# Kernel tuning notes

Measured on AMD Instinct MI355X. Metric: run time of the kernel, lower is better.

## Reference

```python
import jax, jax.numpy as jnp
import numpy as np

B, T, E, A = 512, 64, 1024, 32
S, D, H = 30, 200, 200          # stoch, deter, hidden
SS = D + S                      # state_size = 230
MIN_STD = 0.1
UPDATE_BIAS = -1.0
W_SCALE = 0.05


def setup_inputs() -> dict:
    key = jax.random.key(0)
    ks = jax.random.split(key, 17)
    n = jax.random.normal
    return {
        "embed":       n(ks[0], (B, T, E), jnp.float32),
        "action":      n(ks[1], (B, T, A), jnp.float32),
        "context":     n(ks[2], (B, T, SS), jnp.float32),
        "noise_prior": n(ks[3], (T, B, S), jnp.float32),
        "noise_post":  n(ks[4], (T, B, S), jnp.float32),
        "w_inp":       n(ks[5], (S + SS + A, H), jnp.float32) * W_SCALE,
        "b_inp":       jnp.zeros((H,), jnp.float32),
        "w_gru":       n(ks[6], (H + D, 3 * D), jnp.float32) * W_SCALE,
        "b_gru":       jnp.zeros((3 * D,), jnp.float32),
        "w_img_out":   n(ks[7], (D, H), jnp.float32) * W_SCALE,
        "b_img_out":   jnp.zeros((H,), jnp.float32),
        "w_obs_out":   n(ks[8], (D + E, H), jnp.float32) * W_SCALE,
        "b_obs_out":   jnp.zeros((H,), jnp.float32),
        "w_ims_stat":  n(ks[9], (H, 2 * S), jnp.float32) * W_SCALE,
        "b_ims_stat":  jnp.zeros((2 * S,), jnp.float32),
        "w_obs_stat":  n(ks[10], (H, 2 * S), jnp.float32) * W_SCALE,
        "b_obs_stat":  jnp.zeros((2 * S,), jnp.float32),
    }


def _observe(embed, action, context, noise_prior, noise_post,
             w_inp, b_inp, w_gru, b_gru, w_img_out, b_img_out,
             w_obs_out, b_obs_out, w_ims_stat, b_ims_stat,
             w_obs_stat, b_obs_stat):
    # time-major
    emb_t = jnp.swapaxes(embed, 0, 1)    # [T,B,E]
    act_t = jnp.swapaxes(action, 0, 1)   # [T,B,A]
    ctx_t = jnp.swapaxes(context, 0, 1)  # [T,B,SS]

    def step(carry, xs):
        stoch, deter = carry
        ctx, act, emb, n_p, n_o = xs
        # img_step: input MLP + GRU cell
        x = jnp.concatenate([stoch, ctx, act], -1)
        x = jax.nn.elu(x @ w_inp + b_inp)
        parts = jnp.concatenate([x, deter], -1) @ w_gru + b_gru
        reset, cand, update = jnp.split(parts, 3, -1)
        reset = jax.nn.sigmoid(reset)
        cand = jnp.tanh(reset * cand)
        update = jax.nn.sigmoid(update + UPDATE_BIAS)
        deter_new = update * cand + (1.0 - update) * deter
        # prior stats
        h = jax.nn.elu(deter_new @ w_img_out + b_img_out)
        st = h @ w_ims_stat + b_ims_stat
        pm, ps = jnp.split(st, 2, -1)
        ps = jax.nn.softplus(ps) + MIN_STD
        p_stoch = pm + ps * n_p
        # posterior stats
        ho = jax.nn.elu(jnp.concatenate([deter_new, emb], -1) @ w_obs_out + b_obs_out)
        so = ho @ w_obs_stat + b_obs_stat
        om, os_ = jnp.split(so, 2, -1)
        os_ = jax.nn.softplus(os_) + MIN_STD
        o_stoch = om + os_ * n_o
        out = jnp.concatenate([om, os_, o_stoch, pm, ps, p_stoch, deter_new], -1)
        return (o_stoch, deter_new), out

    carry0 = (jnp.zeros((B, S), embed.dtype), jnp.zeros((B, D), embed.dtype))
    _, ys = jax.lax.scan(step, carry0, (ctx_t, act_t, emb_t, noise_prior, noise_post))
    # ys: [T,B,6S+D] -> [B,T,6S+D]  (post mean/std/stoch, prior mean/std/stoch, deter)
    return jnp.swapaxes(ys, 0, 1)


def reference(embed, action, context, noise_prior, noise_post,
              w_inp, b_inp, w_gru, b_gru, w_img_out, b_img_out,
              w_obs_out, b_obs_out, w_ims_stat, b_ims_stat,
              w_obs_stat, b_obs_stat):
    return _observe(embed, action, context, noise_prior, noise_post,
                    w_inp, b_inp, w_gru, b_gru, w_img_out, b_img_out,
                    w_obs_out, b_obs_out, w_ims_stat, b_ims_stat,
                    w_obs_stat, b_obs_stat)
```

## Files before the change

kernel.cpp:

```cpp
#include <hip/hip_runtime.h>
#include <cstddef>

typedef short short8 __attribute__((ext_vector_type(8)));
typedef float f32x4 __attribute__((ext_vector_type(4)));
typedef unsigned short u16;

#define Bn 512
#define Tn 64
#define En 1024
#define An 32
#define Sn 30
#define Dn 200
#define Hn 200
#define SSn 230
#define OUTC 380

#define U16_WINP  0
#define EL_WINP   66560
#define U16_WGRU  66560
#define EL_WGRU   252928
#define U16_WIMG  319488
#define EL_WIMG   46592
#define U16_WOBSD 366080
#define EL_WOBSD  46592
#define U16_WIMS  412672
#define EL_WIMS   14336
#define U16_WOBSS 427008
#define EL_WOBSS  14336
#define U16_WOBSE 441344
#define EL_WOBSE  212992
#define U16_TOTAL 654336
#define PREOBS_BYTE_OFF 1308672

#define DEV static __device__ __forceinline__

DEV u16 f2bf(float f) {
  union { float f; unsigned u; } v; v.f = f;
  return (u16)((v.u + 0x7FFFu + ((v.u >> 16) & 1u)) >> 16);
}
DEV float bf2f(u16 h) {
  union { unsigned u; float f; } v; v.u = ((unsigned)h) << 16; return v.f;
}
DEV float elu1(float x)  { return x > 0.f ? x : expm1f(x); }
DEV float sigm(float x)  { return 1.f / (1.f + expf(-x)); }
DEV float splus(float x) { return x > 20.f ? x : log1pf(expf(x)); }

DEV void pack_one(const float* src, u16* dst, int li, int KT,
                  int Kr, int Nr, int ldN, int roff) {
  int j = li & 7, lane = (li >> 3) & 63, frag = li >> 9;
  int kt = frag % KT, nt = frag / KT;
  int k = kt * 32 + ((lane >> 4) << 3) + j;
  int n = nt * 16 + (lane & 15);
  float v = (k < Kr && n < Nr) ? src[(size_t)(k + roff) * ldN + n] : 0.f;
  dst[li] = f2bf(v);
}

__global__ __launch_bounds__(256) void k_pack(
    const float* w_inp, const float* w_gru, const float* w_img,
    const float* w_obs, const float* w_ims, const float* w_obss,
    u16* ws) {
  int idx = blockIdx.x * 256 + threadIdx.x;
  if (idx < U16_WGRU)       pack_one(w_inp,  ws + U16_WINP,  idx - U16_WINP, 10, 292, 200, 200, 0);
  else if (idx < U16_WIMG)  pack_one(w_gru,  ws + U16_WGRU,  idx - U16_WGRU, 13, 400, 600, 600, 0);
  else if (idx < U16_WOBSD) pack_one(w_img,  ws + U16_WIMG,  idx - U16_WIMG,  7, 200, 200, 200, 0);
  else if (idx < U16_WIMS)  pack_one(w_obs,  ws + U16_WOBSD, idx - U16_WOBSD, 7, 200, 200, 200, 0);
  else if (idx < U16_WOBSS) pack_one(w_ims,  ws + U16_WIMS,  idx - U16_WIMS,  7, 200,  60,  60, 0);
  else if (idx < U16_WOBSE) pack_one(w_obss, ws + U16_WOBSS, idx - U16_WOBSS, 7, 200,  60,  60, 0);
  else if (idx < U16_TOTAL) pack_one(w_obs,  ws + U16_WOBSE, idx - U16_WOBSE, 32, 1024, 200, 200, 200);
}

__global__ __launch_bounds__(256) void k_preobs(
    const float* __restrict__ emb, const u16* __restrict__ ws,
    float* __restrict__ pre) {
  __shared__ u16 Asm[64 * 72];
  __shared__ short8 Bsm[26 * 64];
  const short8* Wp = (const short8*)(ws + U16_WOBSE);

  int tid = threadIdx.x, wv = tid >> 6, lane = tid & 63;
  int lrow = lane & 15, quad = lane >> 4;
  int m0 = blockIdx.x * 64;
  int t = m0 >> 9, brow0 = m0 & 511;

  f32x4 acc[13];
  const f32x4 z4 = {0.f, 0.f, 0.f, 0.f};
#pragma unroll
  for (int i = 0; i < 13; ++i) acc[i] = z4;

  for (int kc = 0; kc < 16; ++kc) {
    __syncthreads();
#pragma unroll
    for (int q = 0; q < 4; ++q) {
      int i = tid + q * 256;
      int row = i >> 4, c4 = i & 15;
      const float* src = emb + ((size_t)((brow0 + row) * Tn + t)) * En + kc * 64 + c4 * 4;
      float4 v = *(const float4*)src;
      union { u16 h[4]; unsigned long long ll; } p;
      p.h[0] = f2bf(v.x); p.h[1] = f2bf(v.y); p.h[2] = f2bf(v.z); p.h[3] = f2bf(v.w);
      *(unsigned long long*)&Asm[row * 72 + c4 * 4] = p.ll;
    }
    for (int q = 0; q < 7; ++q) {
      int i = tid + q * 256;
      if (i < 1664) {
        int pair = i >> 6, l = i & 63;
        int ktl = pair / 13, nt = pair % 13;
        Bsm[i] = Wp[(nt * 32 + kc * 2 + ktl) * 64 + l];
      }
    }
    __syncthreads();
#pragma unroll
    for (int ktl = 0; ktl < 2; ++ktl) {
      short8 a = *(const short8*)&Asm[(wv * 16 + lrow) * 72 + ktl * 32 + quad * 8];
#pragma unroll
      for (int nt = 0; nt < 13; ++nt)
        acc[nt] = __builtin_amdgcn_mfma_f32_16x16x32_bf16(a, Bsm[(ktl * 13 + nt) * 64 + lane], acc[nt], 0, 0, 0);
    }
  }
#pragma unroll
  for (int nt = 0; nt < 13; ++nt) {
    int col = nt * 16 + lrow;
    if (col < 200) {
#pragma unroll
      for (int r = 0; r < 4; ++r) {
        int m = m0 + wv * 16 + quad * 4 + r;
        pre[(size_t)m * 200 + col] = acc[nt][r];
      }
    }
  }
}

__global__ __launch_bounds__(512, 2) void k_scan(
    const float* __restrict__ g_ctx, const float* __restrict__ g_act,
    const float* __restrict__ g_np, const float* __restrict__ g_no,
    const float* __restrict__ b_inp, const float* __restrict__ b_gru,
    const float* __restrict__ b_img, const float* __restrict__ b_obs,
    const float* __restrict__ b_ims, const float* __restrict__ b_obss,
    const u16* __restrict__ ws, const float* __restrict__ pre,
    float* __restrict__ out) {

  __shared__ u16 gin[16 * 424];
  __shared__ u16 U[16 * 616];
  __shared__ u16 hA[16 * 232];
  __shared__ u16 hoA[16 * 232];
  __shared__ float stp[16 * 66];
  __shared__ float sto[16 * 66];

  const short8* Winp  = (const short8*)(ws + U16_WINP);
  const short8* Wgru  = (const short8*)(ws + U16_WGRU);
  const short8* Wimg  = (const short8*)(ws + U16_WIMG);
  const short8* Wobsd = (const short8*)(ws + U16_WOBSD);
  const short8* Wims  = (const short8*)(ws + U16_WIMS);
  const short8* Wobss = (const short8*)(ws + U16_WOBSS);

  int tid = threadIdx.x, wv = tid >> 6, lane = tid & 63;
  int lrow = lane & 15, quad = lane >> 4;
  int b0 = blockIdx.x * 16;
  const f32x4 z4 = {0.f, 0.f, 0.f, 0.f};

  for (int i = tid; i < 16 * 424; i += 512) gin[i] = 0;
  for (int i = tid; i < 16 * 616; i += 512) U[i] = 0;
  for (int i = tid; i < 16 * 232; i += 512) { hA[i] = 0; hoA[i] = 0; }
  __syncthreads();

  for (int t = 0; t < Tn; ++t) {
    {
      int row = tid >> 5, sub = tid & 31;
      const float* crow = g_ctx + ((size_t)(b0 + row) * Tn + t) * SSn;
      for (int i = sub; i < SSn; i += 32) U[row * 328 + 30 + i] = f2bf(crow[i]);
      const float* arow = g_act + ((size_t)(b0 + row) * Tn + t) * An;
      if (sub < An) U[row * 328 + 260 + sub] = f2bf(arow[sub]);
      if (sub < 28) U[row * 328 + 292 + sub] = 0;
    }
    __syncthreads();

    for (int nt = wv; nt < 13; nt += 8) {
      f32x4 acc = z4;
      const short8* bp = Winp + (size_t)(nt * 10) * 64 + lane;
#pragma unroll
      for (int kt = 0; kt < 10; ++kt) {
        short8 a = *(const short8*)&U[lrow * 328 + kt * 32 + quad * 8];
        acc = __builtin_amdgcn_mfma_f32_16x16x32_bf16(a, bp[kt * 64], acc, 0, 0, 0);
      }
      int col = nt * 16 + lrow;
      if (col < 200) {
        float bias = b_inp[col];
#pragma unroll
        for (int r = 0; r < 4; ++r)
          gin[(quad * 4 + r) * 424 + col] = f2bf(elu1(acc[r] + bias));
      }
    }
    __syncthreads();

    for (int nt = wv; nt < 38; nt += 8) {
      f32x4 acc = z4;
      const short8* bp = Wgru + (size_t)(nt * 13) * 64 + lane;
#pragma unroll
      for (int kt = 0; kt < 13; ++kt) {
        short8 a = *(const short8*)&gin[lrow * 424 + kt * 32 + quad * 8];
        acc = __builtin_amdgcn_mfma_f32_16x16x32_bf16(a, bp[kt * 64], acc, 0, 0, 0);
      }
      int col = nt * 16 + lrow;
      if (col < 600) {
        float bias = b_gru[col];
#pragma unroll
        for (int r = 0; r < 4; ++r)
          U[(quad * 4 + r) * 616 + col] = f2bf(acc[r] + bias);
      }
    }
    __syncthreads();

    for (int i = tid; i < 16 * Dn; i += 512) {
      int row = i / Dn, d = i % Dn;
      float rg = bf2f(U[row * 616 + d]);
      float cg = bf2f(U[row * 616 + 200 + d]);
      float ug = bf2f(U[row * 616 + 400 + d]);
      float dold = bf2f(gin[row * 424 + 200 + d]);
      float rs  = sigm(rg);
      float cnd = tanhf(rs * cg);
      float up  = sigm(ug - 1.f);
      float dn  = up * cnd + (1.f - up) * dold;
      gin[row * 424 + 200 + d] = f2bf(dn);
      __builtin_nontemporal_store(dn, &out[((size_t)(b0 + row) * Tn + t) * OUTC + 180 + d]);
    }
    __syncthreads();

    for (int j = wv; j < 26; j += 8) {
      bool isobs = j >= 13;
      int nt = isobs ? j - 13 : j;
      const short8* bp = (isobs ? Wobsd : Wimg) + (size_t)(nt * 7) * 64 + lane;
      f32x4 acc = z4;
#pragma unroll
      for (int kt = 0; kt < 7; ++kt) {
        short8 a = *(const short8*)&gin[lrow * 424 + 200 + kt * 32 + quad * 8];
        acc = __builtin_amdgcn_mfma_f32_16x16x32_bf16(a, bp[kt * 64], acc, 0, 0, 0);
      }
      int col = nt * 16 + lrow;
      if (col < 200) {
        if (!isobs) {
          float bias = b_img[col];
#pragma unroll
          for (int r = 0; r < 4; ++r)
            hA[(quad * 4 + r) * 232 + col] = f2bf(elu1(acc[r] + bias));
        } else {
          float bias = b_obs[col];
#pragma unroll
          for (int r = 0; r < 4; ++r) {
            int row = quad * 4 + r;
            float po = pre[((size_t)t * Bn + b0 + row) * 200 + col];
            hoA[row * 232 + col] = f2bf(elu1(acc[r] + bias + po));
          }
        }
      }
    }
    __syncthreads();

    {
      bool isobs = wv >= 4;
      int nt = wv & 3;
      const short8* bp = (isobs ? Wobss : Wims) + (size_t)(nt * 7) * 64 + lane;
      const u16* src = isobs ? hoA : hA;
      f32x4 acc = z4;
#pragma unroll
      for (int kt = 0; kt < 7; ++kt) {
        short8 a = *(const short8*)&src[lrow * 232 + kt * 32 + quad * 8];
        acc = __builtin_amdgcn_mfma_f32_16x16x32_bf16(a, bp[kt * 64], acc, 0, 0, 0);
      }
      int col = nt * 16 + lrow;
      if (col < 60) {
        float bias = (isobs ? b_obss : b_ims)[col];
        float* dst = isobs ? sto : stp;
#pragma unroll
        for (int r = 0; r < 4; ++r)
          dst[(quad * 4 + r) * 66 + col] = acc[r] + bias;
      }
    }
    __syncthreads();

    if (tid < 480) {
      int row = tid / 30, s = tid % 30;
      size_t ob = ((size_t)(b0 + row) * Tn + t) * OUTC;
      size_t ni = ((size_t)t * Bn + b0 + row) * Sn + s;
      float pm = stp[row * 66 + s];
      float ps = splus(stp[row * 66 + 30 + s]) + 0.1f;
      float pst = pm + ps * g_np[ni];
      float om = sto[row * 66 + s];
      float os = splus(sto[row * 66 + 30 + s]) + 0.1f;
      float ost = om + os * g_no[ni];
      __builtin_nontemporal_store(om,  &out[ob + s]);
      __builtin_nontemporal_store(os,  &out[ob + 30 + s]);
      __builtin_nontemporal_store(ost, &out[ob + 60 + s]);
      __builtin_nontemporal_store(pm,  &out[ob + 90 + s]);
      __builtin_nontemporal_store(ps,  &out[ob + 120 + s]);
      __builtin_nontemporal_store(pst, &out[ob + 150 + s]);
      U[row * 328 + s] = f2bf(ost);
    }
    __syncthreads();
  }
}

extern "C" void kernel_launch(void* const* d_in, const int* in_sizes, int n_in,
                              void* d_out, int out_size, void* d_ws, size_t ws_size,
                              hipStream_t stream) {
  (void)in_sizes; (void)n_in; (void)out_size; (void)ws_size;
  const float* emb    = (const float*)d_in[0];
  const float* action = (const float*)d_in[1];
  const float* ctx    = (const float*)d_in[2];
  const float* np_    = (const float*)d_in[3];
  const float* no_    = (const float*)d_in[4];
  const float* w_inp  = (const float*)d_in[5];
  const float* b_inp  = (const float*)d_in[6];
  const float* w_gru  = (const float*)d_in[7];
  const float* b_gru  = (const float*)d_in[8];
  const float* w_img  = (const float*)d_in[9];
  const float* b_img  = (const float*)d_in[10];
  const float* w_obs  = (const float*)d_in[11];
  const float* b_obs  = (const float*)d_in[12];
  const float* w_ims  = (const float*)d_in[13];
  const float* b_ims  = (const float*)d_in[14];
  const float* w_obss = (const float*)d_in[15];
  const float* b_obss = (const float*)d_in[16];

  u16*   wsu = (u16*)d_ws;
  float* pre = (float*)((char*)d_ws + PREOBS_BYTE_OFF);
  float* out = (float*)d_out;

  k_pack<<<2556, 256, 0, stream>>>(w_inp, w_gru, w_img, w_obs, w_ims, w_obss, wsu);
  k_preobs<<<512, 256, 0, stream>>>(emb, wsu, pre);
  k_scan<<<32, 512, 0, stream>>>(ctx, action, np_, no_,
                                 b_inp, b_gru, b_img, b_obs, b_ims, b_obss,
                                 wsu, pre, out);
}
```

Before: 1.486 ms.

## Keep scan weights register-resident, fuse GRU gates into MFMA epilogue, prefetch inputs

The recurrent scan kernel now runs 16 waves per block. Each wave loads its slice of every weight matrix into registers once, instead of re-reading the packed weights from global memory at every timestep. The GRU weight packing is interleaved so one wave computes the reset, candidate and update tiles for the same columns, and the gate math runs in the MFMA epilogue, removing the shared-memory gate buffer and a separate elementwise pass. Next-step context and action, noise values and the precomputed observation terms are prefetched into registers early in each step. The trailing barrier is also dropped. The cost is very high register pressure, which risks spills, and several extra barriers per step.

New measurement: 2.572 ms. 73.1% more time.

```diff
diff --git a/kernel.cpp b/kernel.cpp
--- a/kernel.cpp
+++ b/kernel.cpp
@@ -16,23 +16,25 @@
 #define OUTC 380
 
 #define U16_WINP  0
-#define EL_WINP   66560
 #define U16_WGRU  66560
-#define EL_WGRU   252928
-#define U16_WIMG  319488
-#define EL_WIMG   46592
-#define U16_WOBSD 366080
-#define EL_WOBSD  46592
-#define U16_WIMS  412672
-#define EL_WIMS   14336
-#define U16_WOBSS 427008
-#define EL_WOBSS  14336
-#define U16_WOBSE 441344
-#define EL_WOBSE  212992
-#define U16_TOTAL 654336
-#define PREOBS_BYTE_OFF 1308672
+#define U16_WIMG  326144
+#define U16_WOBSD 372736
+#define U16_WIMS  419328
+#define U16_WOBSS 433664
+#define U16_WOBSE 448000
+#define U16_TOTAL 660992
+#define PREOBS_BYTE_OFF 1321984
+
+#define WINP8  0
+#define WGRU8  8320
+#define WIMG8  40768
+#define WOBSD8 46592
+#define WIMS8  52416
+#define WOBSS8 54208
+#define WOBSE8 56000
 
 #define DEV static __device__ __forceinline__
+#define MFMA(a,b,c) __builtin_amdgcn_mfma_f32_16x16x32_bf16((a),(b),(c),0,0,0)
 
 DEV u16 f2bf(float f) {
   union { float f; unsigned u; } v; v.f = f;
@@ -60,13 +62,24 @@
     const float* w_obs, const float* w_ims, const float* w_obss,
     u16* ws) {
   int idx = blockIdx.x * 256 + threadIdx.x;
-  if (idx < U16_WGRU)       pack_one(w_inp,  ws + U16_WINP,  idx - U16_WINP, 10, 292, 200, 200, 0);
-  else if (idx < U16_WIMG)  pack_one(w_gru,  ws + U16_WGRU,  idx - U16_WGRU, 13, 400, 600, 600, 0);
+  if (idx >= U16_TOTAL) return;
+  if (idx < U16_WGRU) {
+    pack_one(w_inp, ws + U16_WINP, idx, 10, 292, 200, 200, 0);
+  } else if (idx < U16_WIMG) {
+    int li = idx - U16_WGRU;
+    int j = li & 7, lane = (li >> 3) & 63, frag = li >> 9;
+    int kt = frag % 13, nt = frag / 13;
+    int k = kt * 32 + ((lane >> 4) << 3) + j;
+    int c = lane & 15;
+    int d = (nt / 3) * 16 + c, p = nt % 3;
+    float v = (k < 400 && d < 200) ? w_gru[(size_t)k * 600 + p * 200 + d] : 0.f;
+    ws[U16_WGRU + li] = f2bf(v);
+  }
   else if (idx < U16_WOBSD) pack_one(w_img,  ws + U16_WIMG,  idx - U16_WIMG,  7, 200, 200, 200, 0);
   else if (idx < U16_WIMS)  pack_one(w_obs,  ws + U16_WOBSD, idx - U16_WOBSD, 7, 200, 200, 200, 0);
   else if (idx < U16_WOBSS) pack_one(w_ims,  ws + U16_WIMS,  idx - U16_WIMS,  7, 200,  60,  60, 0);
   else if (idx < U16_WOBSE) pack_one(w_obss, ws + U16_WOBSS, idx - U16_WOBSS, 7, 200,  60,  60, 0);
-  else if (idx < U16_TOTAL) pack_one(w_obs,  ws + U16_WOBSE, idx - U16_WOBSE, 32, 1024, 200, 200, 200);
+  else                      pack_one(w_obs,  ws + U16_WOBSE, idx - U16_WOBSE, 32, 1024, 200, 200, 200);
 }
 
 __global__ __launch_bounds__(256) void k_preobs(
@@ -112,7 +125,7 @@
       short8 a = *(const short8*)&Asm[(wv * 16 + lrow) * 72 + ktl * 32 + quad * 8];
 #pragma unroll
       for (int nt = 0; nt < 13; ++nt)
-        acc[nt] = __builtin_amdgcn_mfma_f32_16x16x32_bf16(a, Bsm[(ktl * 13 + nt) * 64 + lane], acc[nt], 0, 0, 0);
+        acc[nt] = MFMA(a, Bsm[(ktl * 13 + nt) * 64 + lane], acc[nt]);
     }
   }
 #pragma unroll
@@ -128,7 +141,7 @@
   }
 }
 
-__global__ __launch_bounds__(512, 2) void k_scan(
+__global__ __launch_bounds__(1024, 4) void k_scan(
     const float* __restrict__ g_ctx, const float* __restrict__ g_act,
     const float* __restrict__ g_np, const float* __restrict__ g_no,
     const float* __restrict__ b_inp, const float* __restrict__ b_gru,
@@ -138,162 +151,220 @@
     float* __restrict__ out) {
 
   __shared__ u16 gin[16 * 424];
-  __shared__ u16 U[16 * 616];
+  __shared__ u16 Uin[16 * 344];
   __shared__ u16 hA[16 * 232];
   __shared__ u16 hoA[16 * 232];
   __shared__ float stp[16 * 66];
   __shared__ float sto[16 * 66];
 
-  const short8* Winp  = (const short8*)(ws + U16_WINP);
-  const short8* Wgru  = (const short8*)(ws + U16_WGRU);
-  const short8* Wimg  = (const short8*)(ws + U16_WIMG);
-  const short8* Wobsd = (const short8*)(ws + U16_WOBSD);
-  const short8* Wims  = (const short8*)(ws + U16_WIMS);
-  const short8* Wobss = (const short8*)(ws + U16_WOBSS);
-
-  int tid = threadIdx.x, wv = tid >> 6, lane = tid & 63;
-  int lrow = lane & 15, quad = lane >> 4;
-  int b0 = blockIdx.x * 16;
+  const int tid = threadIdx.x, wv = tid >> 6, lane = tid & 63;
+  const int lrow = lane & 15, quad = lane >> 4;
+  const int b0 = blockIdx.x * 16;
   const f32x4 z4 = {0.f, 0.f, 0.f, 0.f};
-
-  for (int i = tid; i < 16 * 424; i += 512) gin[i] = 0;
-  for (int i = tid; i < 16 * 616; i += 512) U[i] = 0;
-  for (int i = tid; i < 16 * 232; i += 512) { hA[i] = 0; hoA[i] = 0; }
+  const short8* Wb = (const short8*)ws;
+
+  const bool actA  = wv < 13;
+  const bool actB  = wv < 13;
+  const bool actC1 = (wv < 7) || (wv >= 13);
+  const bool actD  = wv >= 8;
+  const int ntA = actA ? wv : 12;
+  const int gB  = actB ? wv : 12;
+  const int j0  = wv;
+  const int j1  = (wv < 7) ? 16 + wv : (wv >= 13 ? 10 + wv : 25);
+  const int eD  = actD ? (wv - 8) : 0;
+
+  short8 fA[10], fB[3][13], fC[2][7], fD[7];
+#pragma unroll
+  for (int kt = 0; kt < 10; ++kt) fA[kt] = Wb[WINP8 + (ntA * 10 + kt) * 64 + lane];
+#pragma unroll
+  for (int p = 0; p < 3; ++p)
+#pragma unroll
+    for (int kt = 0; kt < 13; ++kt)
+      fB[p][kt] = Wb[WGRU8 + ((3 * gB + p) * 13 + kt) * 64 + lane];
+  {
+    int base0 = (j0 < 13) ? (WIMG8 + j0 * 7 * 64) : (WOBSD8 + (j0 - 13) * 7 * 64);
+#pragma unroll
+    for (int kt = 0; kt < 7; ++kt) fC[0][kt] = Wb[base0 + kt * 64 + lane];
+    int base1 = (j1 < 13) ? (WIMG8 + j1 * 7 * 64) : (WOBSD8 + (j1 - 13) * 7 * 64);
+#pragma unroll
+    for (int kt = 0; kt < 7; ++kt) fC[1][kt] = Wb[base1 + kt * 64 + lane];
+    int based = (eD < 4) ? (WIMS8 + eD * 7 * 64) : (WOBSS8 + (eD - 4) * 7 * 64);
+#pragma unroll
+    for (int kt = 0; kt < 7; ++kt) fD[kt] = Wb[based + kt * 64 + lane];
+  }
+
+  const int colA = ntA * 16 + lrow;
+  const float bA = (actA && colA < 200) ? b_inp[colA] : 0.f;
+  const int dcol = gB * 16 + lrow;
+  float bgr = 0.f, bgc = 0.f, bgu = 0.f;
+  if (actB && dcol < 200) { bgr = b_gru[dcol]; bgc = b_gru[200 + dcol]; bgu = b_gru[400 + dcol]; }
+  const int c0 = (j0 < 13 ? j0 : j0 - 13) * 16 + lrow;
+  const float bC0 = (c0 < 200) ? (j0 < 13 ? b_img[c0] : b_obs[c0]) : 0.f;
+  const int c1 = (j1 - 13) * 16 + lrow;
+  const float bC1 = (actC1 && c1 < 200) ? b_obs[c1] : 0.f;
+  const int cD = (eD & 3) * 16 + lrow;
+  const float bD = (actD && cD < 60) ? (eD < 4 ? b_ims[cD] : b_obss[cD]) : 0.f;
+
+  const int crow = tid >> 6;
+  const int ci = tid & 63;
+  const int nrow = tid / 30, ns = tid - nrow * 30;
+
+  for (int i = tid; i < 16 * 424; i += 1024) gin[i] = 0;
+  for (int i = tid; i < 16 * 344; i += 1024) Uin[i] = 0;
+  for (int i = tid; i < 16 * 232; i += 1024) { hA[i] = 0; hoA[i] = 0; }
+
+  float pcx[4]; float pact;
+  {
+    const float* cr = g_ctx + ((size_t)(b0 + crow) * Tn + 0) * SSn;
+#pragma unroll
+    for (int s = 0; s < 4; ++s) { int i = ci + s * 64; pcx[s] = (i < SSn) ? cr[i] : 0.f; }
+    pact = (ci < An) ? g_act[((size_t)(b0 + crow) * Tn + 0) * An + ci] : 0.f;
+  }
   __syncthreads();
 
   for (int t = 0; t < Tn; ++t) {
+#pragma unroll
+    for (int s = 0; s < 4; ++s) {
+      int i = ci + s * 64;
+      if (i < SSn) Uin[crow * 344 + 30 + i] = f2bf(pcx[s]);
+    }
+    if (ci < An) Uin[crow * 344 + 260 + ci] = f2bf(pact);
+
+    float vnp = 0.f, vno = 0.f;
+    if (tid < 480) {
+      size_t ni = ((size_t)t * Bn + b0 + nrow) * Sn + ns;
+      vnp = g_np[ni]; vno = g_no[ni];
+    }
+    float pr0[4] = {0.f, 0.f, 0.f, 0.f}, pr1[4] = {0.f, 0.f, 0.f, 0.f};
+    if (wv >= 13) {
+#pragma unroll
+      for (int r = 0; r < 4; ++r)
+        pr0[r] = pre[((size_t)t * Bn + b0 + quad * 4 + r) * 200 + c0];
+    }
+    if (actC1 && c1 < 200) {
+#pragma unroll
+      for (int r = 0; r < 4; ++r)
+        pr1[r] = pre[((size_t)t * Bn + b0 + quad * 4 + r) * 200 + c1];
+    }
+    if (t + 1 < Tn) {
+      const float* cr = g_ctx + ((size_t)(b0 + crow) * Tn + (t + 1)) * SSn;
+#pragma unroll
+      for (int s = 0; s < 4; ++s) { int i = ci + s * 64; pcx[s] = (i < SSn) ? cr[i] : 0.f; }
+      pact = (ci < An) ? g_act[((size_t)(b0 + crow) * Tn + (t + 1)) * An + ci] : 0.f;
+    }
+    __syncthreads();
+
+    if (actA) {
+      f32x4 acc = z4;
+#pragma unroll
+      for (int kt = 0; kt < 10; ++kt) {
+        short8 a = *(const short8*)&Uin[lrow * 344 + kt * 32 + quad * 8];
+        acc = MFMA(a, fA[kt], acc);
+      }
+      if (colA < 200) {
+#pragma unroll
+        for (int r = 0; r < 4; ++r)
+          gin[(quad * 4 + r) * 424 + colA] = f2bf(elu1(acc[r] + bA));
+      }
+    }
+    __syncthreads();
+
+    short8 ab[13];
+    if (actB) {
+#pragma unroll
+      for (int kt = 0; kt < 13; ++kt)
+        ab[kt] = *(const short8*)&gin[lrow * 424 + kt * 32 + quad * 8];
+    }
+    __syncthreads();
+
+    if (actB) {
+      f32x4 ar = z4, ac_ = z4, au = z4;
+#pragma unroll
+      for (int kt = 0; kt < 13; ++kt) ar  = MFMA(ab[kt], fB[0][kt], ar);
+#pragma unroll
+      for (int kt = 0; kt < 13; ++kt) ac_ = MFMA(ab[kt], fB[1][kt], ac_);
+#pragma unroll
+      for (int kt = 0; kt < 13; ++kt) au  = MFMA(ab[kt], fB[2][kt], au);
+      if (dcol < 200) {
+#pragma unroll
+        for (int r = 0; r < 4; ++r) {
+          int row = quad * 4 + r;
+          float rs   = sigm(ar[r] + bgr);
+          float cnd  = tanhf(rs * (ac_[r] + bgc));
+          float up   = sigm(au[r] + bgu - 1.f);
+          float dold = bf2f(gin[row * 424 + 200 + dcol]);
+          float dn   = up * cnd + (1.f - up) * dold;
+          gin[row * 424 + 200 + dcol] = f2bf(dn);
+          __builtin_nontemporal_store(dn, &out[((size_t)(b0 + row) * Tn + t) * OUTC + 180 + dcol]);
+        }
+      }
+    }
+    __syncthreads();
+
     {
-      int row = tid >> 5, sub = tid & 31;
-      const float* crow = g_ctx + ((size_t)(b0 + row) * Tn + t) * SSn;
-      for (int i = sub; i < SSn; i += 32) U[row * 328 + 30 + i] = f2bf(crow[i]);
-      const float* arow = g_act + ((size_t)(b0 + row) * Tn + t) * An;
-      if (sub < An) U[row * 328 + 260 + sub] = f2bf(arow[sub]);
-      if (sub < 28) U[row * 328 + 292 + sub] = 0;
-    }
-    __syncthreads();
-
-    for (int nt = wv; nt < 13; nt += 8) {
-      f32x4 acc = z4;
-      const short8* bp = Winp + (size_t)(nt * 10) * 64 + lane;
-#pragma unroll
-      for (int kt = 0; kt < 10; ++kt) {
-        short8 a = *(const short8*)&U[lrow * 328 + kt * 32 + quad * 8];
-        acc = __builtin_amdgcn_mfma_f32_16x16x32_bf16(a, bp[kt * 64], acc, 0, 0, 0);
-      }
-      int col = nt * 16 + lrow;
-      if (col < 200) {
-        float bias = b_inp[col];
-#pragma unroll
-        for (int r = 0; r < 4; ++r)
-          gin[(quad * 4 + r) * 424 + col] = f2bf(elu1(acc[r] + bias));
-      }
-    }
-    __syncthreads();
-
-    for (int nt = wv; nt < 38; nt += 8) {
-      f32x4 acc = z4;
-      const short8* bp = Wgru + (size_t)(nt * 13) * 64 + lane;
-#pragma unroll
-      for (int kt = 0; kt < 13; ++kt) {
-        short8 a = *(const short8*)&gin[lrow * 424 + kt * 32 + quad * 8];
-        acc = __builtin_amdgcn_mfma_f32_16x16x32_bf16(a, bp[kt * 64], acc, 0, 0, 0);
-      }
-      int col = nt * 16 + lrow;
-      if (col < 600) {
-        float bias = b_gru[col];
-#pragma unroll
-        for (int r = 0; r < 4; ++r)
-          U[(quad * 4 + r) * 616 + col] = f2bf(acc[r] + bias);
-      }
-    }
-    __syncthreads();
-
-    for (int i = tid; i < 16 * Dn; i += 512) {
-      int row = i / Dn, d = i % Dn;
-      float rg = bf2f(U[row * 616 + d]);
-      float cg = bf2f(U[row * 616 + 200 + d]);
-      float ug = bf2f(U[row * 616 + 400 + d]);
-      float dold = bf2f(gin[row * 424 + 200 + d]);
-      float rs  = sigm(rg);
-      float cnd = tanhf(rs * cg);
-      float up  = sigm(ug - 1.f);
-      float dn  = up * cnd + (1.f - up) * dold;
-      gin[row * 424 + 200 + d] = f2bf(dn);
-      __builtin_nontemporal_store(dn, &out[((size_t)(b0 + row) * Tn + t) * OUTC + 180 + d]);
-    }
-    __syncthreads();
-
-    for (int j = wv; j < 26; j += 8) {
-      bool isobs = j >= 13;
-      int nt = isobs ? j - 13 : j;
-      const short8* bp = (isobs ? Wobsd : Wimg) + (size_t)(nt * 7) * 64 + lane;
-      f32x4 acc = z4;
-#pragma unroll
-      for (int kt = 0; kt < 7; ++kt) {
-        short8 a = *(const short8*)&gin[lrow * 424 + 200 + kt * 32 + quad * 8];
-        acc = __builtin_amdgcn_mfma_f32_16x16x32_bf16(a, bp[kt * 64], acc, 0, 0, 0);
-      }
-      int col = nt * 16 + lrow;
-      if (col < 200) {
-        if (!isobs) {
-          float bias = b_img[col];
+      short8 ad[7];
+#pragma unroll
+      for (int kt = 0; kt < 7; ++kt)
+        ad[kt] = *(const short8*)&gin[lrow * 424 + 200 + kt * 32 + quad * 8];
+      f32x4 a0 = z4;
+#pragma unroll
+      for (int kt = 0; kt < 7; ++kt) a0 = MFMA(ad[kt], fC[0][kt], a0);
+      if (c0 < 200) {
+        if (j0 < 13) {
 #pragma unroll
           for (int r = 0; r < 4; ++r)
-            hA[(quad * 4 + r) * 232 + col] = f2bf(elu1(acc[r] + bias));
+            hA[(quad * 4 + r) * 232 + c0] = f2bf(elu1(a0[r] + bC0));
         } else {
-          float bias = b_obs[col];
-#pragma unroll
-          for (int r = 0; r < 4; ++r) {
-            int row = quad * 4 + r;
-            float po = pre[((size_t)t * Bn + b0 + row) * 200 + col];
-            hoA[row * 232 + col] = f2bf(elu1(acc[r] + bias + po));
-          }
+#pragma unroll
+          for (int r = 0; r < 4; ++r)
+            hoA[(quad * 4 + r) * 232 + c0] = f2bf(elu1(a0[r] + bC0 + pr0[r]));
         }
       }
-    }
-    __syncthreads();
-
-    {
-      bool isobs = wv >= 4;
-      int nt = wv & 3;
-      const short8* bp = (isobs ? Wobss : Wims) + (size_t)(nt * 7) * 64 + lane;
-      const u16* src = isobs ? hoA : hA;
+      if (actC1) {
+        f32x4 a1 = z4;
+#pragma unroll
+        for (int kt = 0; kt < 7; ++kt) a1 = MFMA(ad[kt], fC[1][kt], a1);
+        if (c1 < 200) {
+#pragma unroll
+          for (int r = 0; r < 4; ++r)
+            hoA[(quad * 4 + r) * 232 + c1] = f2bf(elu1(a1[r] + bC1 + pr1[r]));
+        }
+      }
+    }
+    __syncthreads();
+
+    if (actD) {
+      const u16* src = (eD < 4) ? hA : hoA;
       f32x4 acc = z4;
 #pragma unroll
       for (int kt = 0; kt < 7; ++kt) {
         short8 a = *(const short8*)&src[lrow * 232 + kt * 32 + quad * 8];
-        acc = __builtin_amdgcn_mfma_f32_16x16x32_bf16(a, bp[kt * 64], acc, 0, 0, 0);
-      }
-      int col = nt * 16 + lrow;
-      if (col < 60) {
-        float bias = (isobs ? b_obss : b_ims)[col];
-        float* dst = isobs ? sto : stp;
-#pragma unroll
-        for (int r = 0; r < 4; ++r)
-          dst[(quad * 4 + r) * 66 + col] = acc[r] + bias;
+        acc = MFMA(a, fD[kt], acc);
+      }
+      if (cD < 60) {
+        float* dst = (eD < 4) ? stp : sto;
+#pragma unroll
+        for (int r = 0; r < 4; ++r) dst[(quad * 4 + r) * 66 + cD] = acc[r] + bD;
       }
     }
     __syncthreads();
 
     if (tid < 480) {
-      int row = tid / 30, s = tid % 30;
-      size_t ob = ((size_t)(b0 + row) * Tn + t) * OUTC;
-      size_t ni = ((size_t)t * Bn + b0 + row) * Sn + s;
-      float pm = stp[row * 66 + s];
-      float ps = splus(stp[row * 66 + 30 + s]) + 0.1f;
-      float pst = pm + ps * g_np[ni];
-      float om = sto[row * 66 + s];
-      float os = splus(sto[row * 66 + 30 + s]) + 0.1f;
-      float ost = om + os * g_no[ni];
-      __builtin_nontemporal_store(om,  &out[ob + s]);
-      __builtin_nontemporal_store(os,  &out[ob + 30 + s]);
-      __builtin_nontemporal_store(ost, &out[ob + 60 + s]);
-      __builtin_nontemporal_store(pm,  &out[ob + 90 + s]);
-      __builtin_nontemporal_store(ps,  &out[ob + 120 + s]);
-      __builtin_nontemporal_store(pst, &out[ob + 150 + s]);
-      U[row * 328 + s] = f2bf(ost);
-    }
-    __syncthreads();
+      size_t ob = ((size_t)(b0 + nrow) * Tn + t) * OUTC;
+      float pm  = stp[nrow * 66 + ns];
+      float ps  = splus(stp[nrow * 66 + 30 + ns]) + 0.1f;
+      float pst = pm + ps * vnp;
+      float om  = sto[nrow * 66 + ns];
+      float os  = splus(sto[nrow * 66 + 30 + ns]) + 0.1f;
+      float ost = om + os * vno;
+      __builtin_nontemporal_store(om,  &out[ob + ns]);
+      __builtin_nontemporal_store(os,  &out[ob + 30 + ns]);
+      __builtin_nontemporal_store(ost, &out[ob + 60 + ns]);
+      __builtin_nontemporal_store(pm,  &out[ob + 90 + ns]);
+      __builtin_nontemporal_store(ps,  &out[ob + 120 + ns]);
+      __builtin_nontemporal_store(pst, &out[ob + 150 + ns]);
+      Uin[nrow * 344 + ns] = f2bf(ost);
+    }
   }
 }
 
@@ -323,9 +394,9 @@
   float* pre = (float*)((char*)d_ws + PREOBS_BYTE_OFF);
   float* out = (float*)d_out;
 
-  k_pack<<<2556, 256, 0, stream>>>(w_inp, w_gru, w_img, w_obs, w_ims, w_obss, wsu);
+  k_pack<<<2582, 256, 0, stream>>>(w_inp, w_gru, w_img, w_obs, w_ims, w_obss, wsu);
   k_preobs<<<512, 256, 0, stream>>>(emb, wsu, pre);
-  k_scan<<<32, 512, 0, stream>>>(ctx, action, np_, no_,
-                                 b_inp, b_gru, b_img, b_obs, b_ims, b_obss,
-                                 wsu, pre, out);
-}
+  k_scan<<<32, 1024, 0, stream>>>(ctx, action, np_, no_,
+                                  b_inp, b_gru, b_img, b_obs, b_ims, b_obss,
+                                  wsu, pre, out);
+}
```
